# Kernel tuning notes

Measured on AMD Instinct MI355X. Metric: run time of the kernel, lower is better.

Reference implementation:

```python
import jax, jax.numpy as jnp
import numpy as np

B, V, H, L = 2, 256, 128, 3
GROUPS = 32  # GroupNorm32 in the 'normalization' head
EPS = 1e-5


def _layernorm(z, g, b):
    m = jnp.mean(z, -1, keepdims=True)
    v = jnp.var(z, -1, keepdims=True)
    return (z - m) * jax.lax.rsqrt(v + EPS) * g + b


def _forward(x, adj_matrix, emb_type, W_node, b_node, W_eattr, b_eattr, W_ee, b_ee,
             Wu, bu, Wv, bv, Wa, ba, Wb, bb, Wc, bc,
             lnh_g, lnh_b, lne_g, lne_b, plo_g, plo_b, plo_W, plo_bW,
             gn_g, gn_b, W_out, b_out):
    # node embed: Embedding(2,H) lookup -> Linear(H,H)
    h = emb_type[x] @ W_node + b_node                      # B V H
    ea = jnp.transpose(adj_matrix, (0, 2, 3, 1))           # B V V 6
    # edge embed: Linear(6,H) -> Linear(H,H)
    e = (ea @ W_eattr + b_eattr) @ W_ee + b_ee             # B V V H
    # graph = graph[..., -6].long(): binary adjacency channel, no grad
    mask = jax.lax.stop_gradient(ea[..., 0])               # B V V
    for l in range(L):
        h_in, e_in = h, e
        # gated anisotropic GCN layer (DIFUSCO GNNLayer, mode='direct')
        Uh = h @ Wu[l] + bu[l]                             # B V H
        Vh = h @ Wv[l] + bv[l]                             # B V H
        e_new = ((h @ Wa[l] + ba[l])[:, None, :, :]
                 + (h @ Wb[l] + bb[l])[:, :, None, :]
                 + (e @ Wc[l] + bc[l]))                    # B V V H
        gates = jax.nn.sigmoid(e_new) * mask[..., None]    # B V V H
        agg = jnp.einsum('bijh,bjh->bih', gates, Vh)       # gated 'sum' aggregation
        h = jax.nn.relu(_layernorm(Uh + agg, lnh_g[l], lnh_b[l]))
        e = jax.nn.relu(_layernorm(e_new, lne_g[l], lne_b[l]))
        # outer residual (GNNDi.dense_forward) + per_layer_out: LN -> SiLU -> Linear
        h = h_in + h
        e = e_in + (jax.nn.silu(_layernorm(e, plo_g[l], plo_b[l])) @ plo_W[l] + plo_bW[l])
    # head: GroupNorm(32,H) -> ReLU -> Conv2d(H, out_channels, 1) on B H V V
    z = jnp.transpose(e, (0, 3, 1, 2))                     # B H V V
    zg = z.reshape(B, GROUPS, H // GROUPS, V, V)
    mu = jnp.mean(zg, axis=(2, 3, 4), keepdims=True)
    var = jnp.var(zg, axis=(2, 3, 4), keepdims=True)
    z = ((zg - mu) * jax.lax.rsqrt(var + EPS)).reshape(B, H, V, V)
    z = jax.nn.relu(z * gn_g[None, :, None, None] + gn_b[None, :, None, None])
    return jnp.einsum('bchw,oc->bohw', z, W_out) + b_out[None, :, None, None]


def setup_inputs() -> dict:
    key = jax.random.key(0)
    ks = jax.random.split(key, 16)
    nrm = lambda k, s: jax.random.normal(k, s, dtype=jnp.float32) * 0.05
    adj = jnp.concatenate([
        (jax.random.uniform(ks[1], (B, 1, V, V)) < 0.15).astype(jnp.float32),  # channel 0: adjacency
        jax.random.normal(ks[2], (B, 5, V, V), dtype=jnp.float32)], axis=1)
    return {
        'x': jax.random.randint(ks[0], (B, V), 0, 2),
        'adj_matrix': adj,
        'emb_type': nrm(ks[3], (2, H)),
        'W_node': nrm(ks[4], (H, H)), 'b_node': jnp.zeros((H,), jnp.float32),
        'W_eattr': nrm(ks[5], (6, H)), 'b_eattr': jnp.zeros((H,), jnp.float32),
        'W_ee': nrm(ks[6], (H, H)), 'b_ee': jnp.zeros((H,), jnp.float32),
        'Wu': nrm(ks[7], (L, H, H)), 'bu': jnp.zeros((L, H), jnp.float32),
        'Wv': nrm(ks[8], (L, H, H)), 'bv': jnp.zeros((L, H), jnp.float32),
        'Wa': nrm(ks[9], (L, H, H)), 'ba': jnp.zeros((L, H), jnp.float32),
        'Wb': nrm(ks[10], (L, H, H)), 'bb': jnp.zeros((L, H), jnp.float32),
        'Wc': nrm(ks[11], (L, H, H)), 'bc': jnp.zeros((L, H), jnp.float32),
        'lnh_g': jnp.ones((L, H), jnp.float32), 'lnh_b': jnp.zeros((L, H), jnp.float32),
        'lne_g': jnp.ones((L, H), jnp.float32), 'lne_b': jnp.zeros((L, H), jnp.float32),
        'plo_g': jnp.ones((L, H), jnp.float32), 'plo_b': jnp.zeros((L, H), jnp.float32),
        'plo_W': nrm(ks[12], (L, H, H)), 'plo_bW': jnp.zeros((L, H), jnp.float32),
        'gn_g': jnp.ones((H,), jnp.float32), 'gn_b': jnp.zeros((H,), jnp.float32),
        'W_out': nrm(ks[13], (1, H)), 'b_out': jnp.zeros((1,), jnp.float32),
    }


def reference(x, adj_matrix, emb_type, W_node, b_node, W_eattr, b_eattr, W_ee, b_ee,
              Wu, bu, Wv, bv, Wa, ba, Wb, bb, Wc, bc,
              lnh_g, lnh_b, lne_g, lne_b, plo_g, plo_b, plo_W, plo_bW,
              gn_g, gn_b, W_out, b_out):
    return _forward(x, adj_matrix, emb_type, W_node, b_node, W_eattr, b_eattr, W_ee, b_ee,
                    Wu, bu, Wv, bv, Wa, ba, Wb, bb, Wc, bc,
                    lnh_g, lnh_b, lne_g, lne_b, plo_g, plo_b, plo_W, plo_bW,
                    gn_g, gn_b, W_out, b_out)
```

## Files before the change

### kernel.cpp

```cpp
#include <hip/hip_runtime.h>
#include <cstdint>
#include <cstddef>


#define EPSV 1e-5f

typedef __attribute__((ext_vector_type(8))) short short8v;
typedef __attribute__((ext_vector_type(4))) float f32x4;

__device__ __forceinline__ float sigmoidf_(float x) { return 1.f / (1.f + __expf(-x)); }

__device__ __forceinline__ unsigned short f2bf(float x) {
    unsigned int u = __float_as_uint(x);
    unsigned int r = u + 0x7FFFu + ((u >> 16) & 1u);
    return (unsigned short)(r >> 16);
}
__device__ __forceinline__ float bf2f(unsigned short u) {
    return __uint_as_float(((unsigned int)u) << 16);
}
__device__ __forceinline__ unsigned int cvtpk(float a, float b) {
    unsigned int r;
    asm("v_cvt_pk_bf16_f32 %0, %1, %2" : "=v"(r) : "v"(a), "v"(b));
    return r;
}
#define SWZ(row, cb) ((cb) ^ (((row) & 7) << 4))

__global__ void k_prep(const int* __restrict__ x, const float* __restrict__ emb,
                       const float* __restrict__ W_node, const float* __restrict__ b_node,
                       float* __restrict__ h, float* __restrict__ aggB,
                       const float* __restrict__ W_ea, const float* __restrict__ b_ea,
                       const float* __restrict__ W_ee, const float* __restrict__ b_ee,
                       float* __restrict__ Wcb, float* __restrict__ bcb,
                       const float* __restrict__ Wc, const float* __restrict__ PW,
                       unsigned short* __restrict__ WT)
{
    const int blk = blockIdx.x, t = threadIdx.x;
    if (blk < 512) {
        __shared__ float se[128];
        if (t < 128) { se[t] = emb[x[blk]*128 + t]; aggB[blk*128 + t] = 0.f; }
        __syncthreads();
        if (t < 128) {
            float acc = b_node[t];
            for (int k = 0; k < 128; ++k) acc = fmaf(se[k], W_node[k*128+t], acc);
            h[blk*128+t] = acc;
        }
    } else if (blk == 512) {
        if (t < 128) {
            float wc0=0,wc1=0,wc2=0,wc3=0,wc4=0,wc5=0,bv=0;
            for (int m = 0; m < 128; ++m) {
                float we = W_ee[m*128 + t];
                wc0 = fmaf(W_ea[0*128+m], we, wc0);
                wc1 = fmaf(W_ea[1*128+m], we, wc1);
                wc2 = fmaf(W_ea[2*128+m], we, wc2);
                wc3 = fmaf(W_ea[3*128+m], we, wc3);
                wc4 = fmaf(W_ea[4*128+m], we, wc4);
                wc5 = fmaf(W_ea[5*128+m], we, wc5);
                bv  = fmaf(b_ea[m], we, bv);
            }
            Wcb[0*128+t]=wc0; Wcb[1*128+t]=wc1; Wcb[2*128+t]=wc2;
            Wcb[3*128+t]=wc3; Wcb[4*128+t]=wc4; Wcb[5*128+t]=wc5;
            bcb[t] = bv + b_ee[t];
        }
    } else {
        const int m = blk - 513;
        const int l = m >> 1;
        const float* src = (m & 1) ? (PW + (size_t)l*16384) : (Wc + (size_t)l*16384);
        unsigned short* dst = WT + (size_t)m*16384;
        for (int idx = t; idx < 16384; idx += 256) {
            int n = idx >> 7, k = idx & 127;
            dst[idx] = f2bf(src[k*128 + n]);
        }
    }
}

__global__ void k_hgemm(float* __restrict__ h, float* __restrict__ Uh, float* __restrict__ aggB,
    const float* __restrict__ Wu_l, const float* __restrict__ bu_l,
    const float* __restrict__ Wv_l, const float* __restrict__ bv_l,
    const float* __restrict__ Wa_l, const float* __restrict__ ba_l,
    const float* __restrict__ Wb_l, const float* __restrict__ bb_l,
    float* __restrict__ VhT, float* __restrict__ AhT, float* __restrict__ Bh,
    const float* __restrict__ lnh_g, const float* __restrict__ lnh_b, int upd)
{
    __shared__ float sh[128];
    __shared__ float sred[4];
    int blk = blockIdx.x, t = threadIdx.x;
    int b = blk >> 8, v = blk & 255;
    float hv_ = h[blk*128 + t];
    if (upd) {
        float val = Uh[blk*128 + t] + aggB[blk*128 + t];
        aggB[blk*128 + t] = 0.f;
        float s = val, q = val*val;
        #pragma unroll
        for (int off = 32; off; off >>= 1) { s += __shfl_down(s, off); q += __shfl_down(q, off); }
        if ((t & 63) == 0) { sred[t>>6] = s; sred[2 + (t>>6)] = q; }
        __syncthreads();
        s = sred[0] + sred[1]; q = sred[2] + sred[3];
        float mean = s * (1.f/128.f);
        float var  = q * (1.f/128.f) - mean*mean;
        float nv = (val - mean) * rsqrtf(var + EPSV) * lnh_g[t] + lnh_b[t];
        hv_ += fmaxf(nv, 0.f);
        h[blk*128 + t] = hv_;
    }
    sh[t] = hv_;
    __syncthreads();
    float au=bu_l[t], av=bv_l[t], aa=ba_l[t], ab=bb_l[t];
    for (int k = 0; k < 128; ++k) {
        float hv = sh[k];
        au = fmaf(hv, Wu_l[k*128+t], au);
        av = fmaf(hv, Wv_l[k*128+t], av);
        aa = fmaf(hv, Wa_l[k*128+t], aa);
        ab = fmaf(hv, Wb_l[k*128+t], ab);
    }
    Uh[blk*128+t]=au; Bh[blk*128+t]=ab;
    VhT[(size_t)(b*128+t)*256 + v] = av;
    AhT[(size_t)(b*128+t)*256 + v] = aa;
}

template<int EINIT, int DO_AGG, int DO_STATS>
__global__ __launch_bounds__(512, 4) void k_layer(
    unsigned short* __restrict__ e,
    const unsigned short* __restrict__ WcT, const unsigned short* __restrict__ PWT,
    const float* __restrict__ bc_l,
    const float* __restrict__ AhT, const float* __restrict__ Bh,
    const float* __restrict__ VhT, const float* __restrict__ adj,
    const float* __restrict__ lne_g, const float* __restrict__ lne_b,
    const float* __restrict__ plo_g, const float* __restrict__ plo_b,
    const float* __restrict__ pbW_l,
    float* __restrict__ aggB,
    const float* __restrict__ Wcb, const float* __restrict__ bcb,
    float* __restrict__ ggsum, float* __restrict__ ggsq)
{
    __shared__ __align__(16) char sW1[32768];
    __shared__ __align__(16) char sW2[32768];
    __shared__ float sRedA[1024];
    __shared__ float sRedB[256];

    const int t = threadIdx.x;
    const int bi = blockIdx.x >> 1, half = blockIdx.x & 1;
    const int b = bi >> 8, i = bi & 255;
    const int w = t >> 6, lane = t & 63;
    const int lane16 = lane & 15, g = lane >> 4;
    const size_t rowbase = (size_t)bi * 32768;
    const int j0 = half*128 + w*16;
    char* sE = sW1 + w*4096;

    short8v a8[4];
    if (EINIT) {
        float am[6];
        const float* adjp = adj + (size_t)b*393216 + (size_t)i*256 + (j0 + lane16);
        #pragma unroll
        for (int m = 0; m < 6; ++m) am[m] = adjp[(size_t)m*65536];
        unsigned short* erow = &e[rowbase + (size_t)(j0 + lane16)*128];
        #pragma unroll
        for (int kst = 0; kst < 4; ++kst) {
            const int base = kst*32 + g*8;
            float4 v0 = *(const float4*)&bcb[base];
            float4 v1 = *(const float4*)&bcb[base+4];
            float vv[8] = {v0.x, v0.y, v0.z, v0.w, v1.x, v1.y, v1.z, v1.w};
            #pragma unroll
            for (int m = 0; m < 6; ++m) {
                const float4 w0 = *(const float4*)&Wcb[m*128 + base];
                const float4 w1 = *(const float4*)&Wcb[m*128 + base + 4];
                vv[0] = fmaf(am[m], w0.x, vv[0]); vv[1] = fmaf(am[m], w0.y, vv[1]);
                vv[2] = fmaf(am[m], w0.z, vv[2]); vv[3] = fmaf(am[m], w0.w, vv[3]);
                vv[4] = fmaf(am[m], w1.x, vv[4]); vv[5] = fmaf(am[m], w1.y, vv[5]);
                vv[6] = fmaf(am[m], w1.z, vv[6]); vv[7] = fmaf(am[m], w1.w, vv[7]);
            }
            short8v vfr;
            #pragma unroll
            for (int pr = 0; pr < 4; ++pr) {
                const unsigned int p = cvtpk(vv[pr*2], vv[pr*2+1]);
                vfr[pr*2]   = (short)(unsigned short)p;
                vfr[pr*2+1] = (short)(unsigned short)(p >> 16);
            }
            a8[kst] = vfr;
            *(short8v*)&erow[base] = vfr;
        }
    } else {
        const unsigned short* arow = e + rowbase + (size_t)(j0 + lane16)*128 + g*8;
        #pragma unroll
        for (int kst = 0; kst < 4; ++kst)
            a8[kst] = *(const short8v*)&arow[kst*32];
    }

    #pragma unroll
    for (int p = 0; p < 4; ++p) {
        const int idx = t*8 + p*4096;
        const int n = idx >> 7, cb = (idx & 127) << 1;
        *(short8v*)(sW1 + n*256 + SWZ(n, cb)) = *(const short8v*)&WcT[idx];
        *(short8v*)(sW2 + n*256 + SWZ(n, cb)) = *(const short8v*)&PWT[idx];
    }
    __syncthreads();

    f32x4 tv[8];
    float agg[8];
    float s1[4] = {0,0,0,0}, q1[4] = {0,0,0,0};
    const int jb = j0 + g*4;
    float4 mk;
    if (DO_AGG) mk = *(const float4*)&adj[(size_t)b*393216 + (size_t)i*256 + jb];
    const float* mkp = (const float*)&mk;
    #pragma unroll
    for (int nt = 0; nt < 8; ++nt) {
        const int col = nt*16 + lane16;
        f32x4 acc = {0.f,0.f,0.f,0.f};
        #pragma unroll
        for (int kst = 0; kst < 4; ++kst) {
            short8v bfr = *(const short8v*)(sW1 + col*256 + SWZ(col, kst*64 + g*16));
            acc = __builtin_amdgcn_mfma_f32_16x16x32_bf16(a8[kst], bfr, acc, 0, 0, 0);
        }
        const float bcB = bc_l[col] + Bh[bi*128 + col];
        const float4 ah = *(const float4*)&AhT[(size_t)(b*128+col)*256 + jb];
        const float* ahp = (const float*)&ah;
        if (DO_AGG) {
            const float4 vh = *(const float4*)&VhT[(size_t)(b*128+col)*256 + jb];
            const float* vhp = (const float*)&vh;
            float a = 0.f;
            #pragma unroll
            for (int r = 0; r < 4; ++r) {
                float tvl = acc[r] + bcB + ahp[r];
                a = fmaf(mkp[r]*sigmoidf_(tvl), vhp[r], a);
                s1[r] += tvl; q1[r] = fmaf(tvl, tvl, q1[r]);
                tv[nt][r] = tvl;
            }
            agg[nt] = a;
        } else {
            #pragma unroll
            for (int r = 0; r < 4; ++r) {
                float tvl = acc[r] + bcB + ahp[r];
                s1[r] += tvl; q1[r] = fmaf(tvl, tvl, q1[r]);
                tv[nt][r] = tvl;
            }
        }
    }
    float mu1[4], rs1[4];
    #pragma unroll
    for (int r = 0; r < 4; ++r) {
        float s = s1[r], q = q1[r];
        s += __shfl_xor(s,1); q += __shfl_xor(q,1);
        s += __shfl_xor(s,2); q += __shfl_xor(q,2);
        s += __shfl_xor(s,4); q += __shfl_xor(q,4);
        s += __shfl_xor(s,8); q += __shfl_xor(q,8);
        float mu = s*(1.f/128.f);
        mu1[r] = mu; rs1[r] = rsqrtf(q*(1.f/128.f) - mu*mu + EPSV);
    }
    float s2[4] = {0,0,0,0}, q2[4] = {0,0,0,0};
    #pragma unroll
    for (int nt = 0; nt < 8; ++nt) {
        const int col = nt*16 + lane16;
        const float lg = lne_g[col], lb = lne_b[col];
        #pragma unroll
        for (int r = 0; r < 4; ++r) {
            float tp = fmaxf(fmaf((tv[nt][r]-mu1[r])*rs1[r], lg, lb), 0.f);
            tv[nt][r] = tp;
            s2[r] += tp; q2[r] = fmaf(tp, tp, q2[r]);
        }
    }
    float mu2[4], rs2[4];
    #pragma unroll
    for (int r = 0; r < 4; ++r) {
        float s = s2[r], q = q2[r];
        s += __shfl_xor(s,1); q += __shfl_xor(q,1);
        s += __shfl_xor(s,2); q += __shfl_xor(q,2);
        s += __shfl_xor(s,4); q += __shfl_xor(q,4);
        s += __shfl_xor(s,8); q += __shfl_xor(q,8);
        float mu = s*(1.f/128.f);
        mu2[r] = mu; rs2[r] = rsqrtf(q*(1.f/128.f) - mu*mu + EPSV);
    }

    __syncthreads();

    #pragma unroll
    for (int nt = 0; nt < 8; ++nt) {
        const int col = nt*16 + lane16;
        const float pg = plo_g[col], pb = plo_b[col];
        float u[4];
        #pragma unroll
        for (int r = 0; r < 4; ++r) {
            float uu = fmaf((tv[nt][r]-mu2[r])*rs2[r], pg, pb);
            u[r] = uu * sigmoidf_(uu);
        }
        const unsigned int p01 = cvtpk(u[0], u[1]);
        const unsigned int p23 = cvtpk(u[2], u[3]);
        const int r0 = g*4;
        *(unsigned short*)(sE + (r0+0)*256 + SWZ(r0+0, col*2)) = (unsigned short)p01;
        *(unsigned short*)(sE + (r0+1)*256 + SWZ(r0+1, col*2)) = (unsigned short)(p01 >> 16);
        *(unsigned short*)(sE + (r0+2)*256 + SWZ(r0+2, col*2)) = (unsigned short)p23;
        *(unsigned short*)(sE + (r0+3)*256 + SWZ(r0+3, col*2)) = (unsigned short)(p23 >> 16);
    }
    short8v b8[4];
    #pragma unroll
    for (int kst = 0; kst < 4; ++kst)
        b8[kst] = *(const short8v*)(sE + lane16*256 + SWZ(lane16, kst*64 + g*16));

    const int jg = j0 + lane16;
    float gs[8], gq[8];
    #pragma unroll
    for (int nt = 0; nt < 8; ++nt) {
        const int an = nt*16 + lane16;
        f32x4 acc = {0.f,0.f,0.f,0.f};
        #pragma unroll
        for (int kst = 0; kst < 4; ++kst) {
            short8v aw = *(const short8v*)(sW2 + an*256 + SWZ(an, kst*64 + g*16));
            acc = __builtin_amdgcn_mfma_f32_16x16x32_bf16(aw, b8[kst], acc, 0, 0, 0);
        }
        const int n0 = nt*16 + g*4;
        const float4 pw4 = *(const float4*)&pbW_l[n0];
        const float* pwp = (const float*)&pw4;
        unsigned short* ep = &e[rowbase + (size_t)jg*128 + n0];
        const ushort4 ev = *(const ushort4*)ep;
        const float o0 = acc[0] + (pwp[0] + bf2f(ev.x));
        const float o1 = acc[1] + (pwp[1] + bf2f(ev.y));
        const float o2 = acc[2] + (pwp[2] + bf2f(ev.z));
        const float o3 = acc[3] + (pwp[3] + bf2f(ev.w));
        if (DO_STATS) {
            gs[nt] = (o0 + o1) + (o2 + o3);
            gq[nt] = fmaf(o0,o0, fmaf(o1,o1, fmaf(o2,o2, o3*o3)));
        }
        uint2 st;
        st.x = cvtpk(o0, o1);
        st.y = cvtpk(o2, o3);
        *(uint2*)ep = st;
    }

    if (DO_AGG) {
        #pragma unroll
        for (int nt = 0; nt < 8; ++nt) {
            float a = agg[nt];
            a += __shfl_xor(a, 16); a += __shfl_xor(a, 32);
            if (lane < 16) sRedA[w*128 + nt*16 + lane] = a;
        }
        __syncthreads();
        if (t < 128) {
            float S = 0.f;
            #pragma unroll
            for (int k = 0; k < 8; ++k) S += sRedA[k*128 + t];
            atomicAdd(&aggB[bi*128 + t], S);
        }
    }
    if (DO_STATS) {
        #pragma unroll
        for (int nt = 0; nt < 8; ++nt) {
            float a = gs[nt], qq = gq[nt];
            a += __shfl_xor(a, 1); qq += __shfl_xor(qq, 1);
            a += __shfl_xor(a, 2); qq += __shfl_xor(qq, 2);
            a += __shfl_xor(a, 4); qq += __shfl_xor(qq, 4);
            a += __shfl_xor(a, 8); qq += __shfl_xor(qq, 8);
            if (lane16 == 0) {
                sRedA[w*32 + nt*4 + g] = a;
                sRedB[w*32 + nt*4 + g] = qq;
            }
        }
        __syncthreads();
        if (t < 32) {
            float S = 0.f, Q = 0.f;
            #pragma unroll
            for (int k = 0; k < 8; ++k) { S += sRedA[k*32 + t]; Q += sRedB[k*32 + t]; }
            atomicAdd(&ggsum[b*32 + t], S);
            atomicAdd(&ggsq[b*32 + t], Q);
        }
    }
}

__global__ void k_gfin(const float* __restrict__ ggsum, const float* __restrict__ ggsq,
                       float* __restrict__ gmu, float* __restrict__ grs)
{
    int t = threadIdx.x;
    float s = ggsum[t], q = ggsq[t];
    const float invN = 1.f/(4.f*65536.f);
    float mu = s*invN;
    float var = q*invN - mu*mu;
    gmu[t] = mu;
    grs[t] = rsqrtf(var + EPSV);
}

__global__ __launch_bounds__(256) void k_head(
    const unsigned short* __restrict__ e, const float* __restrict__ gmu,
    const float* __restrict__ grs, const float* __restrict__ gn_g,
    const float* __restrict__ gn_b, const float* __restrict__ W_out,
    const float* __restrict__ b_out, float* __restrict__ out)
{
    const int blk = blockIdx.x, t = threadIdx.x;
    const int b = blk >> 8;
    const int ch8 = (t & 15)*8, jgrp = t >> 4;
    float gg[8], gb[8], wo[8];
    #pragma unroll
    for (int c = 0; c < 8; ++c) {
        const int ch = ch8 + c;
        const float mu = gmu[b*32 + (ch>>2)], rs = grs[b*32 + (ch>>2)];
        gg[c] = gn_g[ch]*rs;
        gb[c] = gn_b[ch] - mu*gg[c];
        wo[c] = W_out[ch];
    }
    const float bo = b_out[0];
    const unsigned short* erow = e + (size_t)blk*32768;
    float* orow = out + (size_t)blk*256;
    for (int it = 0; it < 16; ++it) {
        const int j = jgrp*16 + it;
        short8v v = *(const short8v*)&erow[(size_t)j*128 + ch8];
        float p = 0.f;
        #pragma unroll
        for (int c = 0; c < 8; ++c) {
            float f = bf2f((unsigned short)v[c]);
            p = fmaf(fmaxf(fmaf(f, gg[c], gb[c]), 0.f), wo[c], p);
        }
        p += __shfl_xor(p, 1); p += __shfl_xor(p, 2);
        p += __shfl_xor(p, 4); p += __shfl_xor(p, 8);
        if ((t & 15) == 0) orow[j] = p + bo;
    }
}

extern "C" void kernel_launch(void* const* d_in, const int* in_sizes, int n_in,
                              void* d_out, int out_size, void* d_ws, size_t ws_size,
                              hipStream_t stream)
{
    const int*   x      = (const int*)  d_in[0];
    const float* adj    = (const float*)d_in[1];
    const float* emb    = (const float*)d_in[2];
    const float* W_node = (const float*)d_in[3];
    const float* b_node = (const float*)d_in[4];
    const float* W_ea   = (const float*)d_in[5];
    const float* b_ea   = (const float*)d_in[6];
    const float* W_ee   = (const float*)d_in[7];
    const float* b_ee   = (const float*)d_in[8];
    const float* Wu     = (const float*)d_in[9];
    const float* bu     = (const float*)d_in[10];
    const float* Wv     = (const float*)d_in[11];
    const float* bv     = (const float*)d_in[12];
    const float* Wa     = (const float*)d_in[13];
    const float* ba     = (const float*)d_in[14];
    const float* Wb     = (const float*)d_in[15];
    const float* bb     = (const float*)d_in[16];
    const float* Wc     = (const float*)d_in[17];
    const float* bc     = (const float*)d_in[18];
    const float* lnh_g  = (const float*)d_in[19];
    const float* lnh_b  = (const float*)d_in[20];
    const float* lne_g  = (const float*)d_in[21];
    const float* lne_b  = (const float*)d_in[22];
    const float* plo_g  = (const float*)d_in[23];
    const float* plo_b  = (const float*)d_in[24];
    const float* plo_W  = (const float*)d_in[25];
    const float* plo_bW = (const float*)d_in[26];
    const float* gn_g   = (const float*)d_in[27];
    const float* gn_b   = (const float*)d_in[28];
    const float* W_out  = (const float*)d_in[29];
    const float* b_out  = (const float*)d_in[30];
    float* out = (float*)d_out;

    float* ws = (float*)d_ws;
    size_t off = 0;
    unsigned short* e = (unsigned short*)(ws + off); off += 8388608;
    float* h    = ws + off; off += 65536;
    float* Uh   = ws + off; off += 65536;
    float* Bh   = ws + off; off += 65536;
    float* VhT  = ws + off; off += 65536;
    float* AhT  = ws + off; off += 65536;
    float* aggB = ws + off; off += 65536;
    float* Wcb  = ws + off; off += 768;
    float* bcb  = ws + off; off += 128;
    float* ggsum = ws + off; off += 64;
    float* ggsq  = ws + off; off += 64;
    float* gmu  = ws + off; off += 64;
    float* grs  = ws + off; off += 64;
    unsigned short* WT = (unsigned short*)(ws + off); off += 49152;

    k_prep<<<519, 256, 0, stream>>>(x, emb, W_node, b_node, h, aggB,
                                    W_ea, b_ea, W_ee, b_ee, Wcb, bcb,
                                    Wc, plo_W, WT);
    hipMemsetAsync(ggsum, 0, 512, stream);

    for (int l = 0; l < 3; ++l) {
        k_hgemm<<<512, 128, 0, stream>>>(h, Uh, aggB,
            Wu + (size_t)l*16384, bu + l*128,
            Wv + (size_t)l*16384, bv + l*128,
            Wa + (size_t)l*16384, ba + l*128,
            Wb + (size_t)l*16384, bb + l*128,
            VhT, AhT, Bh,
            lnh_g + (l==0?0:(l-1)*128), lnh_b + (l==0?0:(l-1)*128), l > 0 ? 1 : 0);
        const unsigned short* WcT_l = WT + (size_t)(2*l)*16384;
        const unsigned short* PWT_l = WT + (size_t)(2*l+1)*16384;
        if (l == 0) {
            k_layer<1,1,0><<<1024, 512, 0, stream>>>(e, WcT_l, PWT_l,
                bc + l*128, AhT, Bh, VhT, adj,
                lne_g + l*128, lne_b + l*128,
                plo_g + l*128, plo_b + l*128,
                plo_bW + l*128, aggB, Wcb, bcb, ggsum, ggsq);
        } else if (l == 1) {
            k_layer<0,1,0><<<1024, 512, 0, stream>>>(e, WcT_l, PWT_l,
                bc + l*128, AhT, Bh, VhT, adj,
                lne_g + l*128, lne_b + l*128,
                plo_g + l*128, plo_b + l*128,
                plo_bW + l*128, aggB, Wcb, bcb, ggsum, ggsq);
        } else {
            k_layer<0,0,1><<<1024, 512, 0, stream>>>(e, WcT_l, PWT_l,
                bc + l*128, AhT, Bh, VhT, adj,
                lne_g + l*128, lne_b + l*128,
                plo_g + l*128, plo_b + l*128,
                plo_bW + l*128, aggB, Wcb, bcb, ggsum, ggsq);
        }
    }

    k_gfin<<<1, 64, 0, stream>>>(ggsum, ggsq, gmu, grs);
    k_head<<<512, 256, 0, stream>>>(e, gmu, grs, gn_g, gn_b, W_out, b_out, out);
}
```

Measured before the change: 250.3 us.

## Halve k_layer block size and reuse one shared weight buffer for both GEMMs

Each k_layer block now covers 64 edge columns with 256 threads instead of 128 with 512, so the grid doubles to 2048 blocks. The two 32KB shared-memory weight tiles become one buffer: Wc is loaded first and the per-layer-out weight is reloaded into the same space after the first GEMM, behind extra barriers. This halves LDS per block so more blocks can reside per CU. The cost is twice as many global weight loads per edge row, two more syncs, and the launch bound no longer pins occupancy.

```diff
diff --git a/kernel.cpp b/kernel.cpp
--- a/kernel.cpp
+++ b/kernel.cpp
@@ -117,7 +117,7 @@
 }
 
 template<int EINIT, int DO_AGG, int DO_STATS>
-__global__ __launch_bounds__(512, 4) void k_layer(
+__global__ __launch_bounds__(256) void k_layer(
     unsigned short* __restrict__ e,
     const unsigned short* __restrict__ WcT, const unsigned short* __restrict__ PWT,
     const float* __restrict__ bc_l,
@@ -130,19 +130,18 @@
     const float* __restrict__ Wcb, const float* __restrict__ bcb,
     float* __restrict__ ggsum, float* __restrict__ ggsq)
 {
-    __shared__ __align__(16) char sW1[32768];
-    __shared__ __align__(16) char sW2[32768];
-    __shared__ float sRedA[1024];
-    __shared__ float sRedB[256];
+    __shared__ __align__(16) char sW[32768];
+    __shared__ float sRedA[512];
+    __shared__ float sRedB[128];
 
     const int t = threadIdx.x;
-    const int bi = blockIdx.x >> 1, half = blockIdx.x & 1;
+    const int bi = blockIdx.x >> 2, chunk = blockIdx.x & 3;
     const int b = bi >> 8, i = bi & 255;
     const int w = t >> 6, lane = t & 63;
     const int lane16 = lane & 15, g = lane >> 4;
     const size_t rowbase = (size_t)bi * 32768;
-    const int j0 = half*128 + w*16;
-    char* sE = sW1 + w*4096;
+    const int j0 = chunk*64 + w*16;
+    char* sE = sW + w*4096;
 
     short8v a8[4];
     if (EINIT) {
@@ -184,11 +183,10 @@
     }
 
     #pragma unroll
-    for (int p = 0; p < 4; ++p) {
-        const int idx = t*8 + p*4096;
+    for (int p = 0; p < 8; ++p) {
+        const int idx = t*8 + p*2048;
         const int n = idx >> 7, cb = (idx & 127) << 1;
-        *(short8v*)(sW1 + n*256 + SWZ(n, cb)) = *(const short8v*)&WcT[idx];
-        *(short8v*)(sW2 + n*256 + SWZ(n, cb)) = *(const short8v*)&PWT[idx];
+        *(short8v*)(sW + n*256 + SWZ(n, cb)) = *(const short8v*)&WcT[idx];
     }
     __syncthreads();
 
@@ -205,7 +203,7 @@
         f32x4 acc = {0.f,0.f,0.f,0.f};
         #pragma unroll
         for (int kst = 0; kst < 4; ++kst) {
-            short8v bfr = *(const short8v*)(sW1 + col*256 + SWZ(col, kst*64 + g*16));
+            short8v bfr = *(const short8v*)(sW + col*256 + SWZ(col, kst*64 + g*16));
             acc = __builtin_amdgcn_mfma_f32_16x16x32_bf16(a8[kst], bfr, acc, 0, 0, 0);
         }
         const float bcB = bc_l[col] + Bh[bi*128 + col];
@@ -292,6 +290,15 @@
     for (int kst = 0; kst < 4; ++kst)
         b8[kst] = *(const short8v*)(sE + lane16*256 + SWZ(lane16, kst*64 + g*16));
 
+    __syncthreads();
+    #pragma unroll
+    for (int p = 0; p < 8; ++p) {
+        const int idx = t*8 + p*2048;
+        const int n = idx >> 7, cb = (idx & 127) << 1;
+        *(short8v*)(sW + n*256 + SWZ(n, cb)) = *(const short8v*)&PWT[idx];
+    }
+    __syncthreads();
+
     const int jg = j0 + lane16;
     float gs[8], gq[8];
     #pragma unroll
@@ -300,7 +307,7 @@
         f32x4 acc = {0.f,0.f,0.f,0.f};
         #pragma unroll
         for (int kst = 0; kst < 4; ++kst) {
-            short8v aw = *(const short8v*)(sW2 + an*256 + SWZ(an, kst*64 + g*16));
+            short8v aw = *(const short8v*)(sW + an*256 + SWZ(an, kst*64 + g*16));
             acc = __builtin_amdgcn_mfma_f32_16x16x32_bf16(aw, b8[kst], acc, 0, 0, 0);
         }
         const int n0 = nt*16 + g*4;
@@ -331,9 +338,7 @@
         }
         __syncthreads();
         if (t < 128) {
-            float S = 0.f;
-            #pragma unroll
-            for (int k = 0; k < 8; ++k) S += sRedA[k*128 + t];
+            float S = sRedA[t] + sRedA[128+t] + sRedA[256+t] + sRedA[384+t];
             atomicAdd(&aggB[bi*128 + t], S);
         }
     }
@@ -352,9 +357,8 @@
         }
         __syncthreads();
         if (t < 32) {
-            float S = 0.f, Q = 0.f;
-            #pragma unroll
-            for (int k = 0; k < 8; ++k) { S += sRedA[k*32 + t]; Q += sRedB[k*32 + t]; }
+            float S = sRedA[t] + sRedA[32+t] + sRedA[64+t] + sRedA[96+t];
+            float Q = sRedB[t] + sRedB[32+t] + sRedB[64+t] + sRedB[96+t];
             atomicAdd(&ggsum[b*32 + t], S);
             atomicAdd(&ggsq[b*32 + t], Q);
         }
@@ -479,19 +483,19 @@
         const unsigned short* WcT_l = WT + (size_t)(2*l)*16384;
         const unsigned short* PWT_l = WT + (size_t)(2*l+1)*16384;
         if (l == 0) {
-            k_layer<1,1,0><<<1024, 512, 0, stream>>>(e, WcT_l, PWT_l,
+            k_layer<1,1,0><<<2048, 256, 0, stream>>>(e, WcT_l, PWT_l,
                 bc + l*128, AhT, Bh, VhT, adj,
                 lne_g + l*128, lne_b + l*128,
                 plo_g + l*128, plo_b + l*128,
                 plo_bW + l*128, aggB, Wcb, bcb, ggsum, ggsq);
         } else if (l == 1) {
-            k_layer<0,1,0><<<1024, 512, 0, stream>>>(e, WcT_l, PWT_l,
+            k_layer<0,1,0><<<2048, 256, 0, stream>>>(e, WcT_l, PWT_l,
                 bc + l*128, AhT, Bh, VhT, adj,
                 lne_g + l*128, lne_b + l*128,
                 plo_g + l*128, plo_b + l*128,
                 plo_bW + l*128, aggB, Wcb, bcb, ggsum, ggsq);
         } else {
-            k_layer<0,0,1><<<1024, 512, 0, stream>>>(e, WcT_l, PWT_l,
+            k_layer<0,0,1><<<2048, 256, 0, stream>>>(e, WcT_l, PWT_l,
                 bc + l*128, AhT, Bh, VhT, adj,
                 lne_g + l*128, lne_b + l*128,
                 plo_g + l*128, plo_b + l*128,
```

Result: faster. 227.7 us (-9.0%).
